# Kernel optimization log

Hardware: AMD Instinct MI355X
Metric: run time of the kernel (lower is better)

Reference implementation:

```python
import jax, jax.numpy as jnp
import numpy as np

N_NODES = 100000
N_EDGES = 3200000
IN_CH, HID, OUT_CH = 512, 16, 64


def gcn_conv(x, src, dst, W, b, n_nodes):
    """GCNConv: x @ W, then sym-normalized aggregation with self-loops."""
    xw = x @ W  # [N, F_out]
    loop = jnp.arange(n_nodes, dtype=src.dtype)
    s = jnp.concatenate([src, loop])  # sources (messages gathered here)
    d = jnp.concatenate([dst, loop])  # targets (messages scattered here)
    deg = jax.ops.segment_sum(jnp.ones_like(d, dtype=xw.dtype), d, num_segments=n_nodes)
    dinv = jnp.where(deg > 0, jax.lax.rsqrt(deg), 0.0)
    norm = dinv[s] * dinv[d]  # [E+N]
    msgs = xw[s] * norm[:, None]  # gather + scale
    out = jax.ops.segment_sum(msgs, d, num_segments=n_nodes)
    return out + b


def setup_inputs() -> dict:
    key = jax.random.key(0)
    k1, k2, k3, k4, k5 = jax.random.split(key, 5)
    x = jax.random.normal(k1, (N_NODES, IN_CH), dtype=jnp.float32)
    edge_index = jax.random.randint(k2, (2, N_EDGES), 0, N_NODES, dtype=jnp.int32)
    # Glorot-style init for GCNConv linear weights, zero bias (PyG default)
    W1 = jax.random.normal(k3, (IN_CH, HID), dtype=jnp.float32) * (1.0 / np.sqrt(IN_CH))
    b1 = jnp.zeros((HID,), dtype=jnp.float32)
    W2 = jax.random.normal(k4, (HID, OUT_CH), dtype=jnp.float32) * (1.0 / np.sqrt(HID))
    b2 = jnp.zeros((OUT_CH,), dtype=jnp.float32)
    return {"x": x, "edge_index": edge_index, "W1": W1, "b1": b1, "W2": W2, "b2": b2}


def reference(x, edge_index, W1, b1, W2, b2):
    # eval mode: dropout(p=0.5) is identity
    src, dst = edge_index[0], edge_index[1]
    h = gcn_conv(x, src, dst, W1, b1, N_NODES)
    h = jax.nn.relu(h)
    out = gcn_conv(h, src, dst, W2, b2, N_NODES)
    return out
```

## Files before the change

kernel.cpp:

```cpp
#include <hip/hip_runtime.h>

#define N_NODES 100000
#define N_EDGES 3200000
#define IN_CH 512
#define HID 16
#define OUT_CH 64

#define SCAN_BS 256
#define SCAN_CHUNK 1024
#define SCAN_NB ((N_NODES + SCAN_CHUNK - 1) / SCAN_CHUNK)

#define NB1 98
#define CAP1 34816
#define LEAF 64
#define CAP2 2560
#define NLEAF 1563
#define NLEAF_SLOTS (NB1 * 16)
#define BIN1_CHUNK 4096
#define BIN1_BLOCKS ((N_EDGES + BIN1_CHUNK - 1) / BIN1_CHUNK)
#define BIN2_SPLIT 9
#define BIN2_CHUNK 3872


__global__ void k_init_bcur(int* bcur1, int* bcur2) {
    int i = blockIdx.x * blockDim.x + threadIdx.x;
    if (i < NB1) bcur1[i] = i * CAP1;
    if (i < NLEAF_SLOTS) bcur2[i] = i * CAP2;
}


__global__ __launch_bounds__(256) void k_bin1(const int* __restrict__ src,
                                              const int* __restrict__ dst,
                                              int* __restrict__ pairs1,
                                              int* __restrict__ bcur1) {
    __shared__ int cnt[NB1];
    __shared__ int base[NB1];
    const int tid = threadIdx.x;
    const int lo = blockIdx.x * BIN1_CHUNK;
    const int hi = min(lo + BIN1_CHUNK, N_EDGES);
    if (tid < NB1) cnt[tid] = 0;
    __syncthreads();
    for (int i = lo + tid; i < hi; i += 256) {
        int d = __builtin_nontemporal_load(dst + i);
        atomicAdd(&cnt[d >> 10], 1);
    }
    __syncthreads();
    if (tid < NB1 && cnt[tid] > 0) base[tid] = atomicAdd(&bcur1[tid], cnt[tid]);
    __syncthreads();
    if (tid < NB1) cnt[tid] = 0;
    __syncthreads();
    for (int i = lo + tid; i < hi; i += 256) {
        int d = __builtin_nontemporal_load(dst + i);
        int s = __builtin_nontemporal_load(src + i);
        int b = d >> 10;
        int r = atomicAdd(&cnt[b], 1);
        pairs1[base[b] + r] = (s << 10) | (d & 1023);
    }
}


__global__ __launch_bounds__(256) void k_bin2(const int* __restrict__ pairs1,
                                              const int* __restrict__ bcur1,
                                              int* __restrict__ pairs2,
                                              int* __restrict__ bcur2) {
    __shared__ int cnt[16];
    __shared__ int base[16];
    const int b = blockIdx.x / BIN2_SPLIT;
    const int s = blockIdx.x % BIN2_SPLIT;
    const int tid = threadIdx.x;
    const int len = bcur1[b] - b * CAP1;
    const int lo = b * CAP1 + min(s * BIN2_CHUNK, len);
    const int hi = b * CAP1 + min((s + 1) * BIN2_CHUNK, len);
    if (tid < 16) cnt[tid] = 0;
    __syncthreads();
    for (int i = lo + tid; i < hi; i += 256)
        atomicAdd(&cnt[(pairs1[i] & 1023) >> 6], 1);
    __syncthreads();
    if (tid < 16 && cnt[tid] > 0) base[tid] = atomicAdd(&bcur2[b * 16 + tid], cnt[tid]);
    __syncthreads();
    if (tid < 16) cnt[tid] = 0;
    __syncthreads();
    for (int i = lo + tid; i < hi; i += 256) {
        int e = pairs1[i];
        int l = (e & 1023) >> 6;
        int r = atomicAdd(&cnt[l], 1);
        pairs2[base[l] + r] = e;
    }
}


__global__ __launch_bounds__(256) void k_leafcount(const int* __restrict__ pairs2,
                                                   const int* __restrict__ bcur2,
                                                   int* __restrict__ deg) {
    __shared__ int cnt[LEAF];
    const int leaf = blockIdx.x;
    const int tid = threadIdx.x;
    const int base2 = leaf * CAP2;
    const int len = min(bcur2[leaf] - base2, CAP2);
    if (tid < LEAF) cnt[tid] = 0;
    __syncthreads();
    for (int i = tid; i < len; i += 256)
        atomicAdd(&cnt[pairs2[base2 + i] & 63], 1);
    __syncthreads();
    int node = leaf * LEAF + tid;
    if (tid < LEAF && node < N_NODES) deg[node] = 1 + cnt[tid];
}


__global__ void k_scan_partial(const int* __restrict__ deg, int* __restrict__ partials) {
    __shared__ int sm[SCAN_BS];
    int tid = threadIdx.x;
    int base = blockIdx.x * SCAN_CHUNK;
    int s = 0;
    for (int j = 0; j < 4; ++j) {
        int i = base + j * SCAN_BS + tid;
        if (i < N_NODES) s += deg[i] - 1;
    }
    sm[tid] = s;
    __syncthreads();
    for (int st = SCAN_BS / 2; st > 0; st >>= 1) {
        if (tid < st) sm[tid] += sm[tid + st];
        __syncthreads();
    }
    if (tid == 0) partials[blockIdx.x] = sm[0];
}

__global__ void k_scan_offsets(int* partials) {
    __shared__ int sm[128];
    int tid = threadIdx.x;
    int v = (tid < SCAN_NB) ? partials[tid] : 0;
    sm[tid] = v;
    __syncthreads();
    for (int st = 1; st < 128; st <<= 1) {
        int t = (tid >= st) ? sm[tid - st] : 0;
        __syncthreads();
        sm[tid] += t;
        __syncthreads();
    }
    if (tid < SCAN_NB) partials[tid] = sm[tid] - v;
}

__global__ void k_scan_final(const int* __restrict__ deg, const int* __restrict__ partials,
                             int* __restrict__ off, float* __restrict__ dinv) {
    __shared__ int sm[SCAN_BS];
    int tid = threadIdx.x;
    int base = blockIdx.x * SCAN_CHUNK + tid * 4;
    int v[4];
    int s = 0;
    for (int j = 0; j < 4; ++j) {
        int i = base + j;
        v[j] = (i < N_NODES) ? deg[i] - 1 : 0;
        s += v[j];
    }
    sm[tid] = s;
    __syncthreads();
    for (int st = 1; st < SCAN_BS; st <<= 1) {
        int t = (tid >= st) ? sm[tid - st] : 0;
        __syncthreads();
        sm[tid] += t;
        __syncthreads();
    }
    int run = partials[blockIdx.x] + sm[tid] - s;
    for (int j = 0; j < 4; ++j) {
        int i = base + j;
        if (i < N_NODES) {
            off[i] = run;
            dinv[i] = rsqrtf((float)deg[i]);
        }
        run += v[j];
    }
}


__global__ __launch_bounds__(256) void k_scatter2(const int* __restrict__ pairs2,
                                                  const int* __restrict__ bcur2,
                                                  const int* __restrict__ off,
                                                  int* __restrict__ csr) {
    __shared__ int lcur[LEAF];
    __shared__ int buf[CAP2];
    const int leaf = blockIdx.x;
    const int tid = threadIdx.x;
    const int nbase = leaf * LEAF;
    const int obase = off[nbase];
    const int base2 = leaf * CAP2;
    const int len = min(bcur2[leaf] - base2, CAP2);
    if (tid < LEAF) {
        int node = nbase + tid;
        lcur[tid] = (node < N_NODES ? off[node] : 0) - obase;
    }
    __syncthreads();
    for (int i = tid; i < len; i += 256) {
        int e = pairs2[base2 + i];
        int p = atomicAdd(&lcur[e & 63], 1);
        buf[p] = e >> 10;
    }
    __syncthreads();
    for (int i = tid; i < len; i += 256)
        csr[obase + i] = buf[i];
}


#define G1_BS 256
#define G1_NODES 128
#define G1_KT 64
#define G1_STRIDE (G1_KT + 4)

__global__ __launch_bounds__(G1_BS) void k_gemm1(const float* __restrict__ x,
                                                 const float* __restrict__ W1,
                                                 const float* __restrict__ dinv,
                                                 float* __restrict__ y1) {
    __shared__ float xt[G1_NODES * G1_STRIDE];
    __shared__ float wt[G1_KT * HID];
    const int tid = threadIdx.x;
    const int nl = tid >> 2;
    const int cg = tid & 3;
    const int node_base = blockIdx.x * G1_NODES;

    float4 acc0 = {0.f, 0.f, 0.f, 0.f};
    float4 acc1 = {0.f, 0.f, 0.f, 0.f};

    for (int kt = 0; kt < IN_CH; kt += G1_KT) {
        __syncthreads();
        for (int j = 0; j < 8; ++j) {
            int f4 = j * G1_BS + tid;
            int r = f4 >> 4;
            int c4 = f4 & 15;
            int gr = node_base + r;
            float4 v = {0.f, 0.f, 0.f, 0.f};
            if (gr < N_NODES)
                v = *(const float4*)(x + (size_t)gr * IN_CH + kt + c4 * 4);
            *(float4*)(xt + r * G1_STRIDE + c4 * 4) = v;
        }
        {
            int r = tid >> 2;
            int c4 = tid & 3;
            *(float4*)(wt + r * HID + c4 * 4) =
                *(const float4*)(W1 + (size_t)(kt + r) * HID + c4 * 4);
        }
        __syncthreads();

        for (int kk = 0; kk < G1_KT; ++kk) {
            float xv0 = xt[nl * G1_STRIDE + kk];
            float xv1 = xt[(nl + 64) * G1_STRIDE + kk];
            float4 w = *(const float4*)(wt + kk * HID + cg * 4);
            acc0.x += xv0 * w.x; acc0.y += xv0 * w.y;
            acc0.z += xv0 * w.z; acc0.w += xv0 * w.w;
            acc1.x += xv1 * w.x; acc1.y += xv1 * w.y;
            acc1.z += xv1 * w.z; acc1.w += xv1 * w.w;
        }
    }

    int n0 = node_base + nl;
    int n1 = n0 + 64;
    if (n0 < N_NODES) {
        float dv = dinv[n0];
        float4 o = {acc0.x * dv, acc0.y * dv, acc0.z * dv, acc0.w * dv};
        *(float4*)(y1 + (size_t)n0 * HID + cg * 4) = o;
    }
    if (n1 < N_NODES) {
        float dv = dinv[n1];
        float4 o = {acc1.x * dv, acc1.y * dv, acc1.z * dv, acc1.w * dv};
        *(float4*)(y1 + (size_t)n1 * HID + cg * 4) = o;
    }
}


__global__ void k_layer1(const float* __restrict__ y1, const int* __restrict__ off,
                         const int* __restrict__ deg, const int* __restrict__ csr,
                         const float* __restrict__ dinv, const float* __restrict__ b1,
                         float* __restrict__ y2) {
    int t = blockIdx.x * blockDim.x + threadIdx.x;
    int n = t >> 4;
    int c = t & 15;
    int base = off[n];
    int cnt = deg[n] - 1;
    float a0 = 0.f, a1 = 0.f, a2 = 0.f, a3 = 0.f;
    int p = 0;
    for (; p + 4 <= cnt; p += 4) {
        int s0 = csr[base + p + 0];
        int s1 = csr[base + p + 1];
        int s2 = csr[base + p + 2];
        int s3 = csr[base + p + 3];
        a0 += y1[s0 * HID + c];
        a1 += y1[s1 * HID + c];
        a2 += y1[s2 * HID + c];
        a3 += y1[s3 * HID + c];
    }
    for (; p < cnt; ++p) a0 += y1[csr[base + p] * HID + c];
    float acc = (a0 + a1) + (a2 + a3);
    float dv = dinv[n];
    float h = dv * (acc + y1[n * HID + c]) + b1[c];
    h = fmaxf(h, 0.f);
    y2[n * HID + c] = h * dv;
}


__global__ void k_layer2(const float* __restrict__ y2, const int* __restrict__ off,
                         const int* __restrict__ deg, const int* __restrict__ csr,
                         const float* __restrict__ dinv, const float* __restrict__ W2,
                         const float* __restrict__ b2, float* __restrict__ out) {
    __shared__ float w2[HID * OUT_CH];
    __shared__ float bs[OUT_CH];
    int tid = threadIdx.x;
    for (int j = tid; j < HID * OUT_CH; j += blockDim.x) w2[j] = W2[j];
    if (tid < OUT_CH) bs[tid] = b2[tid];
    __syncthreads();

    int t = blockIdx.x * blockDim.x + tid;
    int n = t >> 4;
    int c = t & 15;
    int base = off[n];
    int cnt = deg[n] - 1;
    float a0 = 0.f, a1 = 0.f, a2 = 0.f, a3 = 0.f;
    int p = 0;
    for (; p + 4 <= cnt; p += 4) {
        int s0 = csr[base + p + 0];
        int s1 = csr[base + p + 1];
        int s2 = csr[base + p + 2];
        int s3 = csr[base + p + 3];
        a0 += y2[s0 * HID + c];
        a1 += y2[s1 * HID + c];
        a2 += y2[s2 * HID + c];
        a3 += y2[s3 * HID + c];
    }
    for (; p < cnt; ++p) a0 += y2[csr[base + p] * HID + c];
    float acc = (a0 + a1) + (a2 + a3);
    float z = dinv[n] * (acc + y2[n * HID + c]);

    float4 o = {bs[c * 4 + 0], bs[c * 4 + 1], bs[c * 4 + 2], bs[c * 4 + 3]};
    int lane = tid & 63;
    int gsub = lane >> 4;
    for (int cc = 0; cc < HID; ++cc) {
        float zz = __shfl(z, gsub * 16 + cc, 64);
        float4 w = *(const float4*)(w2 + cc * OUT_CH + c * 4);
        o.x += zz * w.x; o.y += zz * w.y; o.z += zz * w.z; o.w += zz * w.w;
    }
    *(float4*)(out + (size_t)n * OUT_CH + c * 4) = o;
}


extern "C" void kernel_launch(void* const* d_in, const int* in_sizes, int n_in,
                              void* d_out, int out_size, void* d_ws, size_t ws_size,
                              hipStream_t stream) {
    const float* x  = (const float*)d_in[0];
    const int*   ei = (const int*)d_in[1];
    const float* W1 = (const float*)d_in[2];
    const float* b1 = (const float*)d_in[3];
    const float* W2 = (const float*)d_in[4];
    const float* b2 = (const float*)d_in[5];
    float* out = (float*)d_out;

    const int* src = ei;
    const int* dst = ei + N_EDGES;

    char* w = (char*)d_ws;
    const size_t SN = 409600;
    int*   deg      = (int*)(w);
    float* dinv     = (float*)(w + SN);
    int*   off      = (int*)(w + 2 * SN);
    int*   partials = (int*)(w + 3 * SN);
    int*   bcur1    = (int*)(w + 3 * SN + 8192);
    int*   bcur2    = (int*)(w + 3 * SN + 16384);
    char*  regB     = w + 4 * SN;
    int*   pairs1   = (int*)regB;
    int*   csr      = (int*)regB;
    char*  regC     = regB + (size_t)NB1 * CAP1 * 4;
    int*   pairs2   = (int*)regC;
    float* y1       = (float*)regC;
    float* y2       = (float*)(regC + 6553600);

    k_init_bcur<<<(NLEAF_SLOTS + 255) / 256, 256, 0, stream>>>(bcur1, bcur2);
    k_bin1<<<BIN1_BLOCKS, 256, 0, stream>>>(src, dst, pairs1, bcur1);
    k_bin2<<<NB1 * BIN2_SPLIT, 256, 0, stream>>>(pairs1, bcur1, pairs2, bcur2);
    k_leafcount<<<NLEAF, 256, 0, stream>>>(pairs2, bcur2, deg);
    k_scan_partial<<<SCAN_NB, SCAN_BS, 0, stream>>>(deg, partials);
    k_scan_offsets<<<1, 128, 0, stream>>>(partials);
    k_scan_final<<<SCAN_NB, SCAN_BS, 0, stream>>>(deg, partials, off, dinv);
    k_scatter2<<<NLEAF, 256, 0, stream>>>(pairs2, bcur2, off, csr);
    k_gemm1<<<(N_NODES + G1_NODES - 1) / G1_NODES, G1_BS, 0, stream>>>(x, W1, dinv, y1);
    k_layer1<<<(N_NODES * HID) / 256, 256, 0, stream>>>(y1, off, deg, csr, dinv, b1, y2);
    k_layer2<<<(N_NODES * HID) / 256, 256, 0, stream>>>(y2, off, deg, csr, dinv, W2, b2, out);
}
```

Measured before the change: 251.5 us.

## Fuse degree count and scan into scatter, vectorize gathers and GEMM inner loop

```diff
diff --git a/kernel.cpp b/kernel.cpp
--- a/kernel.cpp
+++ b/kernel.cpp
@@ -5,10 +5,6 @@
 #define IN_CH 512
 #define HID 16
 #define OUT_CH 64
-
-#define SCAN_BS 256
-#define SCAN_CHUNK 1024
-#define SCAN_NB ((N_NODES + SCAN_CHUNK - 1) / SCAN_CHUNK)
 
 #define NB1 98
 #define CAP1 34816
@@ -21,6 +17,13 @@
 #define BIN2_SPLIT 9
 #define BIN2_CHUNK 3872
 
+__device__ __forceinline__ float4 f4add(float4 a, float4 b) {
+    return float4{a.x + b.x, a.y + b.y, a.z + b.z, a.w + b.w};
+}
+__device__ __forceinline__ float4 f4fma(float s, float4 w, float4 a) {
+    return float4{a.x + s * w.x, a.y + s * w.y, a.z + s * w.z, a.w + s * w.w};
+}
+
 
 __global__ void k_init_bcur(int* bcur1, int* bcur2) {
     int i = blockIdx.x * blockDim.x + threadIdx.x;
@@ -89,104 +92,68 @@
 }
 
 
-__global__ __launch_bounds__(256) void k_leafcount(const int* __restrict__ pairs2,
-                                                   const int* __restrict__ bcur2,
-                                                   int* __restrict__ deg) {
-    __shared__ int cnt[LEAF];
-    const int leaf = blockIdx.x;
-    const int tid = threadIdx.x;
-    const int base2 = leaf * CAP2;
-    const int len = min(bcur2[leaf] - base2, CAP2);
-    if (tid < LEAF) cnt[tid] = 0;
-    __syncthreads();
-    for (int i = tid; i < len; i += 256)
-        atomicAdd(&cnt[pairs2[base2 + i] & 63], 1);
-    __syncthreads();
-    int node = leaf * LEAF + tid;
-    if (tid < LEAF && node < N_NODES) deg[node] = 1 + cnt[tid];
-}
-
-
-__global__ void k_scan_partial(const int* __restrict__ deg, int* __restrict__ partials) {
-    __shared__ int sm[SCAN_BS];
-    int tid = threadIdx.x;
-    int base = blockIdx.x * SCAN_CHUNK;
-    int s = 0;
-    for (int j = 0; j < 4; ++j) {
-        int i = base + j * SCAN_BS + tid;
-        if (i < N_NODES) s += deg[i] - 1;
-    }
-    sm[tid] = s;
-    __syncthreads();
-    for (int st = SCAN_BS / 2; st > 0; st >>= 1) {
-        if (tid < st) sm[tid] += sm[tid + st];
-        __syncthreads();
-    }
-    if (tid == 0) partials[blockIdx.x] = sm[0];
-}
-
-__global__ void k_scan_offsets(int* partials) {
-    __shared__ int sm[128];
-    int tid = threadIdx.x;
-    int v = (tid < SCAN_NB) ? partials[tid] : 0;
-    sm[tid] = v;
-    __syncthreads();
-    for (int st = 1; st < 128; st <<= 1) {
-        int t = (tid >= st) ? sm[tid - st] : 0;
-        __syncthreads();
-        sm[tid] += t;
-        __syncthreads();
-    }
-    if (tid < SCAN_NB) partials[tid] = sm[tid] - v;
-}
-
-__global__ void k_scan_final(const int* __restrict__ deg, const int* __restrict__ partials,
-                             int* __restrict__ off, float* __restrict__ dinv) {
-    __shared__ int sm[SCAN_BS];
-    int tid = threadIdx.x;
-    int base = blockIdx.x * SCAN_CHUNK + tid * 4;
-    int v[4];
-    int s = 0;
-    for (int j = 0; j < 4; ++j) {
-        int i = base + j;
-        v[j] = (i < N_NODES) ? deg[i] - 1 : 0;
-        s += v[j];
-    }
-    sm[tid] = s;
-    __syncthreads();
-    for (int st = 1; st < SCAN_BS; st <<= 1) {
-        int t = (tid >= st) ? sm[tid - st] : 0;
-        __syncthreads();
-        sm[tid] += t;
-        __syncthreads();
-    }
-    int run = partials[blockIdx.x] + sm[tid] - s;
-    for (int j = 0; j < 4; ++j) {
-        int i = base + j;
-        if (i < N_NODES) {
-            off[i] = run;
-            dinv[i] = rsqrtf((float)deg[i]);
-        }
-        run += v[j];
+__global__ __launch_bounds__(256) void k_leafscan(const int* __restrict__ bcur2,
+                                                  int* __restrict__ leafoff) {
+    __shared__ int sm[256];
+    __shared__ int carry;
+    const int tid = threadIdx.x;
+    if (tid == 0) carry = 0;
+    __syncthreads();
+    for (int r = 0; r < (NLEAF_SLOTS + 255) / 256; ++r) {
+        int idx = r * 256 + tid;
+        int v = (idx < NLEAF_SLOTS) ? (bcur2[idx] - idx * CAP2) : 0;
+        sm[tid] = v;
+        __syncthreads();
+        for (int st = 1; st < 256; st <<= 1) {
+            int t = (tid >= st) ? sm[tid - st] : 0;
+            __syncthreads();
+            sm[tid] += t;
+            __syncthreads();
+        }
+        if (idx < NLEAF_SLOTS) leafoff[idx] = carry + sm[tid] - v;
+        int tot = sm[255];
+        __syncthreads();
+        if (tid == 0) carry += tot;
+        __syncthreads();
     }
 }
 
 
 __global__ __launch_bounds__(256) void k_scatter2(const int* __restrict__ pairs2,
                                                   const int* __restrict__ bcur2,
-                                                  const int* __restrict__ off,
+                                                  const int* __restrict__ leafoff,
+                                                  int* __restrict__ off,
+                                                  int* __restrict__ deg,
+                                                  float* __restrict__ dinv,
                                                   int* __restrict__ csr) {
+    __shared__ int cnt[LEAF];
     __shared__ int lcur[LEAF];
     __shared__ int buf[CAP2];
     const int leaf = blockIdx.x;
     const int tid = threadIdx.x;
-    const int nbase = leaf * LEAF;
-    const int obase = off[nbase];
     const int base2 = leaf * CAP2;
     const int len = min(bcur2[leaf] - base2, CAP2);
+    const int obase = leafoff[leaf];
+    if (tid < LEAF) cnt[tid] = 0;
+    __syncthreads();
+    for (int i = tid; i < len; i += 256)
+        atomicAdd(&cnt[pairs2[base2 + i] & 63], 1);
+    __syncthreads();
     if (tid < LEAF) {
-        int node = nbase + tid;
-        lcur[tid] = (node < N_NODES ? off[node] : 0) - obase;
+        int v = cnt[tid];
+        int s = v;
+        for (int d = 1; d < LEAF; d <<= 1) {
+            int t = __shfl_up(s, d, 64);
+            if (tid >= d) s += t;
+        }
+        int excl = s - v;
+        lcur[tid] = excl;
+        int node = leaf * LEAF + tid;
+        if (node < N_NODES) {
+            off[node] = obase + excl;
+            deg[node] = 1 + v;
+            dinv[node] = rsqrtf((float)(1 + v));
+        }
     }
     __syncthreads();
     for (int i = tid; i < len; i += 256) {
@@ -239,14 +206,17 @@
         }
         __syncthreads();
 
-        for (int kk = 0; kk < G1_KT; ++kk) {
-            float xv0 = xt[nl * G1_STRIDE + kk];
-            float xv1 = xt[(nl + 64) * G1_STRIDE + kk];
-            float4 w = *(const float4*)(wt + kk * HID + cg * 4);
-            acc0.x += xv0 * w.x; acc0.y += xv0 * w.y;
-            acc0.z += xv0 * w.z; acc0.w += xv0 * w.w;
-            acc1.x += xv1 * w.x; acc1.y += xv1 * w.y;
-            acc1.z += xv1 * w.z; acc1.w += xv1 * w.w;
+        for (int kk = 0; kk < G1_KT; kk += 4) {
+            float4 x0 = *(const float4*)(xt + nl * G1_STRIDE + kk);
+            float4 x1 = *(const float4*)(xt + (nl + 64) * G1_STRIDE + kk);
+            float4 w0 = *(const float4*)(wt + (kk + 0) * HID + cg * 4);
+            float4 w1 = *(const float4*)(wt + (kk + 1) * HID + cg * 4);
+            float4 w2 = *(const float4*)(wt + (kk + 2) * HID + cg * 4);
+            float4 w3 = *(const float4*)(wt + (kk + 3) * HID + cg * 4);
+            acc0 = f4fma(x0.x, w0, acc0); acc0 = f4fma(x0.y, w1, acc0);
+            acc0 = f4fma(x0.z, w2, acc0); acc0 = f4fma(x0.w, w3, acc0);
+            acc1 = f4fma(x1.x, w0, acc1); acc1 = f4fma(x1.y, w1, acc1);
+            acc1 = f4fma(x1.z, w2, acc1); acc1 = f4fma(x1.w, w3, acc1);
         }
     }
 
@@ -265,77 +235,114 @@
 }
 
 
-__global__ void k_layer1(const float* __restrict__ y1, const int* __restrict__ off,
-                         const int* __restrict__ deg, const int* __restrict__ csr,
-                         const float* __restrict__ dinv, const float* __restrict__ b1,
-                         float* __restrict__ y2) {
+__global__ __launch_bounds__(256) void k_layer1(const float* __restrict__ y1,
+                                                const int* __restrict__ off,
+                                                const int* __restrict__ deg,
+                                                const int* __restrict__ csr,
+                                                const float* __restrict__ dinv,
+                                                const float* __restrict__ b1,
+                                                float* __restrict__ y2) {
     int t = blockIdx.x * blockDim.x + threadIdx.x;
-    int n = t >> 4;
-    int c = t & 15;
+    int n = t >> 2;
+    int cg = t & 3;
+    if (n >= N_NODES) return;
     int base = off[n];
     int cnt = deg[n] - 1;
-    float a0 = 0.f, a1 = 0.f, a2 = 0.f, a3 = 0.f;
+    float4 a0 = {0,0,0,0}, a1 = {0,0,0,0}, a2 = {0,0,0,0}, a3 = {0,0,0,0};
     int p = 0;
     for (; p + 4 <= cnt; p += 4) {
         int s0 = csr[base + p + 0];
         int s1 = csr[base + p + 1];
         int s2 = csr[base + p + 2];
         int s3 = csr[base + p + 3];
-        a0 += y1[s0 * HID + c];
-        a1 += y1[s1 * HID + c];
-        a2 += y1[s2 * HID + c];
-        a3 += y1[s3 * HID + c];
-    }
-    for (; p < cnt; ++p) a0 += y1[csr[base + p] * HID + c];
-    float acc = (a0 + a1) + (a2 + a3);
+        a0 = f4add(a0, *(const float4*)(y1 + (size_t)s0 * HID + cg * 4));
+        a1 = f4add(a1, *(const float4*)(y1 + (size_t)s1 * HID + cg * 4));
+        a2 = f4add(a2, *(const float4*)(y1 + (size_t)s2 * HID + cg * 4));
+        a3 = f4add(a3, *(const float4*)(y1 + (size_t)s3 * HID + cg * 4));
+    }
+    for (; p < cnt; ++p)
+        a0 = f4add(a0, *(const float4*)(y1 + (size_t)csr[base + p] * HID + cg * 4));
+    float4 acc = f4add(f4add(a0, a1), f4add(a2, a3));
     float dv = dinv[n];
-    float h = dv * (acc + y1[n * HID + c]) + b1[c];
-    h = fmaxf(h, 0.f);
-    y2[n * HID + c] = h * dv;
-}
-
-
-__global__ void k_layer2(const float* __restrict__ y2, const int* __restrict__ off,
-                         const int* __restrict__ deg, const int* __restrict__ csr,
-                         const float* __restrict__ dinv, const float* __restrict__ W2,
-                         const float* __restrict__ b2, float* __restrict__ out) {
+    float4 self = *(const float4*)(y1 + (size_t)n * HID + cg * 4);
+    float4 b = ((const float4*)b1)[cg];
+    float4 h;
+    h.x = fmaxf(dv * (acc.x + self.x) + b.x, 0.f) * dv;
+    h.y = fmaxf(dv * (acc.y + self.y) + b.y, 0.f) * dv;
+    h.z = fmaxf(dv * (acc.z + self.z) + b.z, 0.f) * dv;
+    h.w = fmaxf(dv * (acc.w + self.w) + b.w, 0.f) * dv;
+    *(float4*)(y2 + (size_t)n * HID + cg * 4) = h;
+}
+
+
+__global__ __launch_bounds__(256) void k_layer2(const float* __restrict__ y2,
+                                                const int* __restrict__ off,
+                                                const int* __restrict__ deg,
+                                                const int* __restrict__ csr,
+                                                const float* __restrict__ dinv,
+                                                const float* __restrict__ W2,
+                                                const float* __restrict__ b2,
+                                                float* __restrict__ out) {
     __shared__ float w2[HID * OUT_CH];
     __shared__ float bs[OUT_CH];
     int tid = threadIdx.x;
-    for (int j = tid; j < HID * OUT_CH; j += blockDim.x) w2[j] = W2[j];
+    for (int j = tid; j < HID * OUT_CH; j += 256) w2[j] = W2[j];
     if (tid < OUT_CH) bs[tid] = b2[tid];
     __syncthreads();
 
     int t = blockIdx.x * blockDim.x + tid;
-    int n = t >> 4;
-    int c = t & 15;
+    int n = t >> 2;
+    int cg = t & 3;
+    if (n >= N_NODES) return;
     int base = off[n];
     int cnt = deg[n] - 1;
-    float a0 = 0.f, a1 = 0.f, a2 = 0.f, a3 = 0.f;
+    float4 a0 = {0,0,0,0}, a1 = {0,0,0,0}, a2 = {0,0,0,0}, a3 = {0,0,0,0};
     int p = 0;
     for (; p + 4 <= cnt; p += 4) {
         int s0 = csr[base + p + 0];
         int s1 = csr[base + p + 1];
         int s2 = csr[base + p + 2];
         int s3 = csr[base + p + 3];
-        a0 += y2[s0 * HID + c];
-        a1 += y2[s1 * HID + c];
-        a2 += y2[s2 * HID + c];
-        a3 += y2[s3 * HID + c];
-    }
-    for (; p < cnt; ++p) a0 += y2[csr[base + p] * HID + c];
-    float acc = (a0 + a1) + (a2 + a3);
-    float z = dinv[n] * (acc + y2[n * HID + c]);
-
-    float4 o = {bs[c * 4 + 0], bs[c * 4 + 1], bs[c * 4 + 2], bs[c * 4 + 3]};
+        a0 = f4add(a0, *(const float4*)(y2 + (size_t)s0 * HID + cg * 4));
+        a1 = f4add(a1, *(const float4*)(y2 + (size_t)s1 * HID + cg * 4));
+        a2 = f4add(a2, *(const float4*)(y2 + (size_t)s2 * HID + cg * 4));
+        a3 = f4add(a3, *(const float4*)(y2 + (size_t)s3 * HID + cg * 4));
+    }
+    for (; p < cnt; ++p)
+        a0 = f4add(a0, *(const float4*)(y2 + (size_t)csr[base + p] * HID + cg * 4));
+    float4 acc = f4add(f4add(a0, a1), f4add(a2, a3));
+    float dv = dinv[n];
+    float4 self = *(const float4*)(y2 + (size_t)n * HID + cg * 4);
+    float4 z4 = {dv * (acc.x + self.x), dv * (acc.y + self.y),
+                 dv * (acc.z + self.z), dv * (acc.w + self.w)};
+
     int lane = tid & 63;
-    int gsub = lane >> 4;
+    int lbase = lane & ~3;
+    float z[16];
+    for (int j = 0; j < 4; ++j) {
+        z[j * 4 + 0] = __shfl(z4.x, lbase + j, 64);
+        z[j * 4 + 1] = __shfl(z4.y, lbase + j, 64);
+        z[j * 4 + 2] = __shfl(z4.z, lbase + j, 64);
+        z[j * 4 + 3] = __shfl(z4.w, lbase + j, 64);
+    }
+
+    float4 o0 = ((const float4*)bs)[cg * 4 + 0];
+    float4 o1 = ((const float4*)bs)[cg * 4 + 1];
+    float4 o2 = ((const float4*)bs)[cg * 4 + 2];
+    float4 o3 = ((const float4*)bs)[cg * 4 + 3];
     for (int cc = 0; cc < HID; ++cc) {
-        float zz = __shfl(z, gsub * 16 + cc, 64);
-        float4 w = *(const float4*)(w2 + cc * OUT_CH + c * 4);
-        o.x += zz * w.x; o.y += zz * w.y; o.z += zz * w.z; o.w += zz * w.w;
-    }
-    *(float4*)(out + (size_t)n * OUT_CH + c * 4) = o;
+        const float* wr = w2 + cc * OUT_CH + cg * 16;
+        float zz = z[cc];
+        o0 = f4fma(zz, *(const float4*)(wr + 0), o0);
+        o1 = f4fma(zz, *(const float4*)(wr + 4), o1);
+        o2 = f4fma(zz, *(const float4*)(wr + 8), o2);
+        o3 = f4fma(zz, *(const float4*)(wr + 12), o3);
+    }
+    float* orow = out + (size_t)n * OUT_CH + cg * 16;
+    *(float4*)(orow + 0) = o0;
+    *(float4*)(orow + 4) = o1;
+    *(float4*)(orow + 8) = o2;
+    *(float4*)(orow + 12) = o3;
 }
 
 
@@ -358,9 +365,9 @@
     int*   deg      = (int*)(w);
     float* dinv     = (float*)(w + SN);
     int*   off      = (int*)(w + 2 * SN);
-    int*   partials = (int*)(w + 3 * SN);
-    int*   bcur1    = (int*)(w + 3 * SN + 8192);
-    int*   bcur2    = (int*)(w + 3 * SN + 16384);
+    int*   bcur1    = (int*)(w + 3 * SN);
+    int*   bcur2    = (int*)(w + 3 * SN + 8192);
+    int*   leafoff  = (int*)(w + 3 * SN + 16384);
     char*  regB     = w + 4 * SN;
     int*   pairs1   = (int*)regB;
     int*   csr      = (int*)regB;
@@ -372,12 +379,9 @@
     k_init_bcur<<<(NLEAF_SLOTS + 255) / 256, 256, 0, stream>>>(bcur1, bcur2);
     k_bin1<<<BIN1_BLOCKS, 256, 0, stream>>>(src, dst, pairs1, bcur1);
     k_bin2<<<NB1 * BIN2_SPLIT, 256, 0, stream>>>(pairs1, bcur1, pairs2, bcur2);
-    k_leafcount<<<NLEAF, 256, 0, stream>>>(pairs2, bcur2, deg);
-    k_scan_partial<<<SCAN_NB, SCAN_BS, 0, stream>>>(deg, partials);
-    k_scan_offsets<<<1, 128, 0, stream>>>(partials);
-    k_scan_final<<<SCAN_NB, SCAN_BS, 0, stream>>>(deg, partials, off, dinv);
-    k_scatter2<<<NLEAF, 256, 0, stream>>>(pairs2, bcur2, off, csr);
+    k_leafscan<<<1, 256, 0, stream>>>(bcur2, leafoff);
+    k_scatter2<<<NLEAF, 256, 0, stream>>>(pairs2, bcur2, leafoff, off, deg, dinv, csr);
     k_gemm1<<<(N_NODES + G1_NODES - 1) / G1_NODES, G1_BS, 0, stream>>>(x, W1, dinv, y1);
-    k_layer1<<<(N_NODES * HID) / 256, 256, 0, stream>>>(y1, off, deg, csr, dinv, b1, y2);
-    k_layer2<<<(N_NODES * HID) / 256, 256, 0, stream>>>(y2, off, deg, csr, dinv, W2, b2, out);
-}
+    k_layer1<<<(N_NODES * 4 + 255) / 256, 256, 0, stream>>>(y1, off, deg, csr, dinv, b1, y2);
+    k_layer2<<<(N_NODES * 4 + 255) / 256, 256, 0, stream>>>(y2, off, deg, csr, dinv, W2, b2, out);
+}
```

New measurement: 248.5 us. No clear change (-1.2%).
